# Performance work log

Hardware: AMD Instinct MI355X
Metric: run time of the kernel (lower is better)

The kernel has to match this reference:

```python
import jax, jax.numpy as jnp
import numpy as np

E = 8          # moe_num_experts
F = 4096       # ffn_hidden_size
D = 2048       # d_model
TOP_K = 2


def setup_inputs() -> dict:
    key = jax.random.key(0)
    k_x, k_r, k_w1, k_v1, k_w2 = jax.random.split(key, 5)
    scale = 0.02  # ~ normal initializer scale
    x = jax.random.normal(k_x, (2, 2048, D), dtype=jnp.float32)
    router_w = jax.random.normal(k_r, (D, E), dtype=jnp.float32) * scale
    w1 = jax.random.normal(k_w1, (E * F, D), dtype=jnp.float32) * scale
    v1 = jax.random.normal(k_v1, (E * F, D), dtype=jnp.float32) * scale
    w2 = jax.random.normal(k_w2, (E * F, D), dtype=jnp.float32) * scale
    return {"x": x, "router_w": router_w, "w1": w1, "v1": v1, "w2": w2}


def reference(x, router_w, w1, v1, w2):
    # --- Router: dense logits -> softmax (fp32) -> top-k -> L1 normalize ---
    logits = jnp.einsum("bsd,de->bse", x.astype(jnp.float32), router_w)
    weights = jax.nn.softmax(logits, axis=-1)                       # [B,S,E]
    top_weights, top_experts = jax.lax.top_k(weights, TOP_K)        # [B,S,K]
    # moe_normalize_expert_weights = 1 -> L1 norm
    top_weights = top_weights / jnp.sum(jnp.abs(top_weights), axis=-1, keepdims=True)
    top_weights = top_weights.astype(x.dtype)

    # --- Experts: dense per-expert GLU, masked combine (faithful to source) ---
    w1r = w1.reshape(E, F, D)
    v1r = v1.reshape(E, F, D)
    w2r = w2.reshape(E, F, D)
    out = jnp.zeros_like(x)
    for e in range(E):  # fixed small structural loop over experts
        x1 = jnp.einsum("bsd,fd->bsf", x, w1r[e])
        x2 = jnp.einsum("bsd,fd->bsf", x, v1r[e])
        h = jax.nn.silu(x1) * x2                                    # GLU
        y = jnp.einsum("bsf,fd->bsd", h, w2r[e])
        coef = jnp.sum((top_experts == e) * top_weights, axis=-1)[:, :, None]
        out = out + coef * y
    return out
```

## Files before the change

kernel.cpp:

```cpp
#include <hip/hip_runtime.h>
#include <cstdio>
#include <cstdint>

typedef _Float16 f16;
typedef _Float16 f16x8 __attribute__((ext_vector_type(8)));
typedef float f32x4 __attribute__((ext_vector_type(4)));

#define D_MODEL 2048
#define FFN     4096
#define FFN2    8192
#define NEXP    8
#define NTOK    4096
#define NENT    (NTOK*2)
#define BM      256
#define BN      256
#define BK      64
#define KSPLIT  4
#define KCHUNK  (FFN / KSPLIT)
#define MAX_ROWS  10240
#define MAX_TILES 40

__device__ __forceinline__ void gload_lds16(const void* g, void* l) {
  __builtin_amdgcn_global_load_lds(
      (const __attribute__((address_space(1))) void*)g,
      (__attribute__((address_space(3))) void*)l, 16, 0, 0);
}

template<int N> __device__ __forceinline__ void waitvm() {
  if constexpr (N == 0) asm volatile("s_waitcnt vmcnt(0)" ::: "memory");
  else if constexpr (N == 2) asm volatile("s_waitcnt vmcnt(2)" ::: "memory");
  else if constexpr (N == 4) asm volatile("s_waitcnt vmcnt(4)" ::: "memory");
  else if constexpr (N == 6) asm volatile("s_waitcnt vmcnt(6)" ::: "memory");
}

template<int LD>
__device__ __forceinline__ void stageA(const f16* aT, int k0, f16* AS, int mh, int tid) {
#pragma unroll
  for (int s = 0; s < 2; s++) {
    int o = s*8192 + tid*16;
    int rl = o >> 7;
    int ce = ((o & 127) ^ ((rl & 7) << 4)) >> 1;
    int arow = s*128 + mh*64 + (rl & 63);
    gload_lds16(aT + (size_t)arow * LD + k0 + ce,
                (char*)AS + mh*16384 + s*8192 + (tid & ~63)*16);
  }
}

template<int LD>
__device__ __forceinline__ void stageB(const f16* bT, int k0, f16* BS, int nh, int tid) {
#pragma unroll
  for (int s = 0; s < 2; s++) {
    int o = s*8192 + tid*16;
    int rl = o >> 7;
    int ce = ((o & 127) ^ ((rl & 7) << 4)) >> 1;
    int crow = (rl >> 5)*64 + nh*32 + (rl & 31);
    gload_lds16(bT + (size_t)crow * LD + k0 + ce,
                (char*)BS + nh*16384 + s*8192 + (tid & ~63)*16);
  }
}

__device__ __forceinline__ f16x8 fragLd(const f16* S, int row, int lane, int ks) {
  int kb = ks*64 + (lane >> 4)*16;
  int off = (row*128 + kb) ^ ((row & 7) << 4);
  return *(const f16x8*)((const char*)S + off);
}

template<int LD, int V0, int V1, int V3, bool SB0, bool SB1, bool SA1, bool SA0>
__device__ __forceinline__ void tile4(
    const f16* aT, const f16* bT, int k1, int k2,
    f16* ASc, f16* BSc, f16* ASn, f16* BSn,
    f32x4 (&acc)[8][4], f16x8 (&aF)[4][2], f16x8 (&bF)[2][2][2],
    int tid, int lane, int wrM, int wcN) {
#pragma unroll
  for (int mf = 0; mf < 4; mf++)
#pragma unroll
    for (int ks = 0; ks < 2; ks++)
      aF[mf][ks] = fragLd(ASc, wrM*64 + mf*16 + (lane & 15), lane, ks);
#pragma unroll
  for (int nf = 0; nf < 2; nf++)
#pragma unroll
    for (int ks = 0; ks < 2; ks++)
      bF[0][nf][ks] = fragLd(BSc, wcN*32 + nf*16 + (lane & 15), lane, ks);
  if constexpr (SB0) stageB<LD>(bT, k1, BSn, 0, tid);
  __builtin_amdgcn_s_barrier();
  __builtin_amdgcn_s_setprio(1);
#pragma unroll
  for (int mf = 0; mf < 4; mf++)
#pragma unroll
    for (int nf = 0; nf < 2; nf++)
#pragma unroll
      for (int ks = 0; ks < 2; ks++)
        acc[mf][nf] = __builtin_amdgcn_mfma_f32_16x16x32_f16(aF[mf][ks], bF[0][nf][ks], acc[mf][nf], 0, 0, 0);
  __builtin_amdgcn_s_setprio(0);
  waitvm<V0>();
  __builtin_amdgcn_s_barrier();
#pragma unroll
  for (int nf = 0; nf < 2; nf++)
#pragma unroll
    for (int ks = 0; ks < 2; ks++)
      bF[1][nf][ks] = fragLd(BSc, 128 + wcN*32 + nf*16 + (lane & 15), lane, ks);
  if constexpr (SB1) stageB<LD>(bT, k1, BSn, 1, tid);
  __builtin_amdgcn_s_barrier();
  __builtin_amdgcn_s_setprio(1);
#pragma unroll
  for (int mf = 0; mf < 4; mf++)
#pragma unroll
    for (int nf = 0; nf < 2; nf++)
#pragma unroll
      for (int ks = 0; ks < 2; ks++)
        acc[mf][2+nf] = __builtin_amdgcn_mfma_f32_16x16x32_f16(aF[mf][ks], bF[1][nf][ks], acc[mf][2+nf], 0, 0, 0);
  __builtin_amdgcn_s_setprio(0);
  waitvm<V1>();
  __builtin_amdgcn_s_barrier();
#pragma unroll
  for (int mf = 0; mf < 4; mf++)
#pragma unroll
    for (int ks = 0; ks < 2; ks++)
      aF[mf][ks] = fragLd(ASc, 128 + wrM*64 + mf*16 + (lane & 15), lane, ks);
  if constexpr (SA1) stageA<LD>(aT, k1, ASn, 1, tid);
  __builtin_amdgcn_s_barrier();
  __builtin_amdgcn_s_setprio(1);
#pragma unroll
  for (int mf = 0; mf < 4; mf++)
#pragma unroll
    for (int nf = 0; nf < 2; nf++)
#pragma unroll
      for (int ks = 0; ks < 2; ks++)
        acc[4+mf][nf] = __builtin_amdgcn_mfma_f32_16x16x32_f16(aF[mf][ks], bF[0][nf][ks], acc[4+mf][nf], 0, 0, 0);
  __builtin_amdgcn_s_setprio(0);
  __builtin_amdgcn_s_barrier();
  if constexpr (SA0) stageA<LD>(aT, k2, ASc, 0, tid);
  __builtin_amdgcn_s_barrier();
  __builtin_amdgcn_s_setprio(1);
#pragma unroll
  for (int mf = 0; mf < 4; mf++)
#pragma unroll
    for (int nf = 0; nf < 2; nf++)
#pragma unroll
      for (int ks = 0; ks < 2; ks++)
        acc[4+mf][2+nf] = __builtin_amdgcn_mfma_f32_16x16x32_f16(aF[mf][ks], bF[1][nf][ks], acc[4+mf][2+nf], 0, 0, 0);
  __builtin_amdgcn_s_setprio(0);
  waitvm<V3>();
  __builtin_amdgcn_s_barrier();
}


__global__ void zero_counts_kernel(int* counts) {
  if (threadIdx.x < NEXP) counts[threadIdx.x] = 0;
}

__global__ __launch_bounds__(64) void router_kernel(
    const float* __restrict__ x, const float* __restrict__ rw,
    int* counts, int* te, float* tw, int* trank) {
  int t = blockIdx.x;
  int lane = threadIdx.x;
  float acc[8] = {0.f,0.f,0.f,0.f,0.f,0.f,0.f,0.f};
  const float* xr = x + (size_t)t * D_MODEL;
  for (int d = lane; d < D_MODEL; d += 64) {
    float xv = xr[d];
    const float4* r4 = (const float4*)(rw + (size_t)d * NEXP);
    float4 a = r4[0], b = r4[1];
    acc[0] += xv*a.x; acc[1] += xv*a.y; acc[2] += xv*a.z; acc[3] += xv*a.w;
    acc[4] += xv*b.x; acc[5] += xv*b.y; acc[6] += xv*b.z; acc[7] += xv*b.w;
  }
#pragma unroll
  for (int off = 32; off > 0; off >>= 1) {
#pragma unroll
    for (int e = 0; e < 8; e++) acc[e] += __shfl_down(acc[e], off);
  }
  if (lane == 0) {
    int e0 = 0;
#pragma unroll
    for (int e = 1; e < 8; e++) if (acc[e] > acc[e0]) e0 = e;
    int e1 = (e0 == 0) ? 1 : 0;
#pragma unroll
    for (int e = 0; e < 8; e++) if (e != e0 && acc[e] > acc[e1]) e1 = e;
    float c0 = 1.0f / (1.0f + expf(acc[e1] - acc[e0]));
    float c1 = 1.0f - c0;
    int r0 = atomicAdd(&counts[e0], 1);
    int r1 = atomicAdd(&counts[e1], 1);
    te[t*2] = e0; te[t*2+1] = e1;
    tw[t*2] = c0; tw[t*2+1] = c1;
    trank[t*2] = r0; trank[t*2+1] = r1;
  }
}

__global__ void sched_kernel(const int* counts, int* offsets, int4* sched, int* nT) {
  if (threadIdx.x != 0 || blockIdx.x != 0) return;
  int off = 0, n = 0;
  for (int e = 0; e < NEXP; e++) {
    offsets[e] = off;
    int cnt = counts[e];
    int nt = (cnt + BM - 1) / BM;
    for (int i = 0; i < nt; i++) {
      sched[n] = make_int4(e, off + i*BM, min(BM, cnt - i*BM), 0);
      n++;
    }
    off += nt * BM;
  }
  offsets[NEXP] = off;
  *nT = n;
}

__global__ __launch_bounds__(256) void gather_kernel(
    const float* __restrict__ x, const int* __restrict__ te,
    const float* __restrict__ tw, const int* __restrict__ trank,
    const int* __restrict__ offsets, f16* __restrict__ xg,
    int* __restrict__ token_of, float* __restrict__ coefs) {
  int i = blockIdx.x;
  int t = i >> 1;
  int e = te[i];
  int slot = offsets[e] + trank[i];
  if (threadIdx.x == 0) { token_of[slot] = t; coefs[slot] = tw[i]; }
  const float4* src = (const float4*)(x + (size_t)t * D_MODEL);
  f16x8* dst = (f16x8*)(xg + (size_t)slot * D_MODEL);
  for (int j = threadIdx.x; j < D_MODEL/8; j += 256) {
    float4 v0 = src[j*2], v1 = src[j*2+1];
    f16x8 h;
    h[0]=(f16)v0.x; h[1]=(f16)v0.y; h[2]=(f16)v0.z; h[3]=(f16)v0.w;
    h[4]=(f16)v1.x; h[5]=(f16)v1.y; h[6]=(f16)v1.z; h[7]=(f16)v1.w;
    dst[j] = h;
  }
}

__global__ __launch_bounds__(256) void convert_ileave_kernel(
    const float* __restrict__ src, f16* __restrict__ dst, int parity) {
  int n8 = NEXP*FFN*D_MODEL/8;
  int stride = gridDim.x * 256;
  for (int i = blockIdx.x*256 + threadIdx.x; i < n8; i += stride) {
    int d8 = i & (D_MODEL/8 - 1);
    int fr_glob = i >> 8;
    int e = fr_glob >> 12;
    int fr = fr_glob & (FFN - 1);
    int cr = ((fr >> 4)*2 + parity)*16 + (fr & 15);
    float4 v0 = ((const float4*)src)[(size_t)i*2];
    float4 v1 = ((const float4*)src)[(size_t)i*2 + 1];
    f16x8 h;
    h[0]=(f16)v0.x; h[1]=(f16)v0.y; h[2]=(f16)v0.z; h[3]=(f16)v0.w;
    h[4]=(f16)v1.x; h[5]=(f16)v1.y; h[6]=(f16)v1.z; h[7]=(f16)v1.w;
    ((f16x8*)dst)[((size_t)e*FFN2 + cr)*(D_MODEL/8) + d8] = h;
  }
}

__global__ __launch_bounds__(256) void transpose_w2_kernel(
    const float* __restrict__ w2, f16* __restrict__ w2t) {
  __shared__ float tl[64][65];
  int e = blockIdx.z;
  int d0 = blockIdx.x * 64, f0 = blockIdx.y * 64;
  const float* src = w2 + (size_t)e * FFN * D_MODEL;
  int tid = threadIdx.x;
  int fr = tid >> 4, c4 = (tid & 15) * 4;
#pragma unroll
  for (int rr = 0; rr < 4; rr++) {
    float4 v = *(const float4*)(src + (size_t)(f0 + fr + rr*16) * D_MODEL + d0 + c4);
    tl[fr + rr*16][c4+0] = v.x; tl[fr + rr*16][c4+1] = v.y;
    tl[fr + rr*16][c4+2] = v.z; tl[fr + rr*16][c4+3] = v.w;
  }
  __syncthreads();
  int dr = tid >> 2, fg = (tid & 3) * 16;
  f16* dst = w2t + (size_t)e * D_MODEL * FFN + (size_t)(d0 + dr) * FFN + f0 + fg;
  f16 tmp[16];
#pragma unroll
  for (int j = 0; j < 16; j++) tmp[j] = (f16)tl[fg + j][dr];
  *(float4*)(dst)     = *(float4*)(tmp);
  *(float4*)(dst + 8) = *(float4*)(tmp + 8);
}

__global__ __launch_bounds__(512, 2) void phaseA_kernel(
    const f16* __restrict__ xg, const f16* __restrict__ w12h,
    f16* __restrict__ hbuf, const int4* __restrict__ sched, const int* __restrict__ nT) {
  int tile = blockIdx.y;
  if (tile >= *nT) return;
  int4 sc = sched[tile];
  int e = sc.x, row0 = sc.y;
  int fc0 = blockIdx.x * BN;

  __shared__ f16 AS[2][BM*BK];
  __shared__ f16 BS[2][BN*BK];

  int tid = threadIdx.x, lane = tid & 63, wid = tid >> 6;
  int wrM = wid >> 2, wcN = wid & 3;

  const f16* aT = xg  + (size_t)row0 * D_MODEL;
  const f16* bT = w12h + (size_t)e * FFN2 * D_MODEL + (size_t)fc0 * D_MODEL;

  f32x4 acc[8][4]; f16x8 aF[4][2]; f16x8 bF[2][2][2];
  f32x4 z4 = {0.f,0.f,0.f,0.f};
#pragma unroll
  for (int m = 0; m < 8; m++)
#pragma unroll
    for (int n = 0; n < 4; n++) acc[m][n] = z4;

  stageA<D_MODEL>(aT, 0, AS[0], 0, tid);
  stageB<D_MODEL>(bT, 0, BS[0], 0, tid);
  stageB<D_MODEL>(bT, 0, BS[0], 1, tid);
  stageA<D_MODEL>(aT, 0, AS[0], 1, tid);
  stageA<D_MODEL>(aT, BK, AS[1], 0, tid);
  waitvm<6>();
  __builtin_amdgcn_s_barrier();

  constexpr int NTILES = D_MODEL / BK;
  for (int t = 0; t + 2 < NTILES; t++) {
    int b = t & 1;
    tile4<D_MODEL,6,6,6,true,true,true,true>(aT, bT, (t+1)*BK, (t+2)*BK,
        AS[b], BS[b], AS[b^1], BS[b^1], acc, aF, bF, tid, lane, wrM, wcN);
  }
  { int b = (NTILES-2) & 1;
    tile4<D_MODEL,6,6,4,true,true,true,false>(aT, bT, (NTILES-1)*BK, 0,
        AS[b], BS[b], AS[b^1], BS[b^1], acc, aF, bF, tid, lane, wrM, wcN); }
  { int b = (NTILES-1) & 1;
    tile4<D_MODEL,2,0,-1,false,false,false,false>(aT, bT, 0, 0,
        AS[b], BS[b], AS[b^1], BS[b^1], acc, aF, bF, tid, lane, wrM, wcN); }

  int i15 = lane & 15, l4 = lane >> 4;
#pragma unroll
  for (int m = 0; m < 8; m++) {
    int rowl = wrM*128 + (m>>2)*64 + (m&3)*16 + l4*4;
#pragma unroll
    for (int nh = 0; nh < 2; nh++) {
      int f = (fc0 >> 1) + wcN*32 + nh*16 + i15;
      f16* hb = hbuf + (size_t)(row0 + rowl) * FFN + f;
#pragma unroll
      for (int q = 0; q < 4; q++) {
        float x1 = acc[m][nh*2+0][q], x2 = acc[m][nh*2+1][q];
        float hv = x1 / (1.0f + __expf(-x1)) * x2;
        hb[(size_t)q * FFN] = (f16)hv;
      }
    }
  }
}

__global__ __launch_bounds__(512, 2) void phaseB_kernel(
    const f16* __restrict__ hbuf, const f16* __restrict__ w2t,
    f16* __restrict__ yb0, f16* __restrict__ ybR,
    const int4* __restrict__ sched, const int* __restrict__ nT) {
  int tile = blockIdx.y;
  if (tile >= *nT) return;
  int4 sc = sched[tile];
  int e = sc.x, row0 = sc.y;
  int dc0 = blockIdx.x * BN;
  int z = blockIdx.z;

  __shared__ f16 AS[2][BM*BK];
  __shared__ f16 BS[2][BN*BK];

  int tid = threadIdx.x, lane = tid & 63, wid = tid >> 6;
  int wrM = wid >> 2, wcN = wid & 3;

  const f16* aT = hbuf + (size_t)row0 * FFN + z * KCHUNK;
  const f16* bT = w2t + (size_t)e * D_MODEL * FFN + (size_t)dc0 * FFN + z * KCHUNK;

  f32x4 acc[8][4]; f16x8 aF[4][2]; f16x8 bF[2][2][2];
  f32x4 z4 = {0.f,0.f,0.f,0.f};
#pragma unroll
  for (int m = 0; m < 8; m++)
#pragma unroll
    for (int n = 0; n < 4; n++) acc[m][n] = z4;

  stageA<FFN>(aT, 0, AS[0], 0, tid);
  stageB<FFN>(bT, 0, BS[0], 0, tid);
  stageB<FFN>(bT, 0, BS[0], 1, tid);
  stageA<FFN>(aT, 0, AS[0], 1, tid);
  stageA<FFN>(aT, BK, AS[1], 0, tid);
  waitvm<6>();
  __builtin_amdgcn_s_barrier();

  constexpr int NTILES = KCHUNK / BK;
  for (int t = 0; t + 2 < NTILES; t++) {
    int b = t & 1;
    tile4<FFN,6,6,6,true,true,true,true>(aT, bT, (t+1)*BK, (t+2)*BK,
        AS[b], BS[b], AS[b^1], BS[b^1], acc, aF, bF, tid, lane, wrM, wcN);
  }
  { int b = (NTILES-2) & 1;
    tile4<FFN,6,6,4,true,true,true,false>(aT, bT, (NTILES-1)*BK, 0,
        AS[b], BS[b], AS[b^1], BS[b^1], acc, aF, bF, tid, lane, wrM, wcN); }
  { int b = (NTILES-1) & 1;
    tile4<FFN,2,0,-1,false,false,false,false>(aT, bT, 0, 0,
        AS[b], BS[b], AS[b^1], BS[b^1], acc, aF, bF, tid, lane, wrM, wcN); }

  f16* yb = (z == 0) ? yb0 : (ybR + (size_t)(z-1) * MAX_ROWS * D_MODEL);
  int i15 = lane & 15, l4 = lane >> 4;
#pragma unroll
  for (int m = 0; m < 8; m++) {
#pragma unroll
    for (int q = 0; q < 4; q++) {
      int rl = wrM*128 + (m>>2)*64 + (m&3)*16 + l4*4 + q;
      f16* yrow = yb + (size_t)(row0 + rl) * D_MODEL + dc0 + wcN*64;
#pragma unroll
      for (int n = 0; n < 4; n++)
        yrow[(n>>1)*32 + (n&1)*16 + i15] = (f16)acc[m][n][q];
    }
  }
}

__global__ __launch_bounds__(256) void combine_kernel(
    const f16* __restrict__ yb0, const f16* __restrict__ ybR,
    const int* __restrict__ te, const float* __restrict__ tw,
    const int* __restrict__ trank, const int* __restrict__ offsets,
    float* __restrict__ out) {
  int t = blockIdx.x;
  int d8 = threadIdx.x;
  int s0 = offsets[te[2*t]]   + trank[2*t];
  int s1 = offsets[te[2*t+1]] + trank[2*t+1];
  float w0 = tw[2*t], w1 = tw[2*t+1];
  float sum[8] = {0.f,0.f,0.f,0.f,0.f,0.f,0.f,0.f};
#pragma unroll
  for (int z = 0; z < KSPLIT; z++) {
    const f16* yb = (z == 0) ? yb0 : (ybR + (size_t)(z-1) * MAX_ROWS * D_MODEL);
    f16x8 a = ((const f16x8*)(yb + (size_t)s0 * D_MODEL))[d8];
    f16x8 b = ((const f16x8*)(yb + (size_t)s1 * D_MODEL))[d8];
#pragma unroll
    for (int j = 0; j < 8; j++) sum[j] += w0 * (float)a[j] + w1 * (float)b[j];
  }
  float* o = out + (size_t)t * D_MODEL + d8*8;
  float4 o0 = {sum[0], sum[1], sum[2], sum[3]};
  float4 o1 = {sum[4], sum[5], sum[6], sum[7]};
  ((float4*)o)[0] = o0;
  ((float4*)o)[1] = o1;
}

extern "C" void kernel_launch(void* const* d_in, const int* in_sizes, int n_in,
                              void* d_out, int out_size, void* d_ws, size_t ws_size,
                              hipStream_t stream) {
  const float* x  = (const float*)d_in[0];
  const float* rw = (const float*)d_in[1];
  const float* w1 = (const float*)d_in[2];
  const float* v1 = (const float*)d_in[3];
  const float* w2 = (const float*)d_in[4];
  float* out = (float*)d_out;

  char* p = (char*)d_ws;
  auto alloc = [&](size_t bytes) {
    char* r = p;
    p += (bytes + 255) & ~(size_t)255;
    return r;
  };
  int*   counts   = (int*)  alloc(NEXP * 4);
  int*   nT       = (int*)  alloc(4);
  int*   offsets  = (int*)  alloc((NEXP + 1) * 4);
  int*   te       = (int*)  alloc(NENT * 4);
  float* tw       = (float*)alloc(NENT * 4);
  int*   trank    = (int*)  alloc(NENT * 4);
  int*   token_of = (int*)  alloc(MAX_ROWS * 4);
  float* coefs    = (float*)alloc(MAX_ROWS * 4);
  int4*  sched    = (int4*) alloc(MAX_TILES * 16);
  f16*   xg       = (f16*)  alloc((size_t)MAX_ROWS * D_MODEL * 2);
  f16*   hbuf     = (f16*)  alloc((size_t)MAX_ROWS * FFN * 2);
  f16*   w12h     = (f16*)  alloc((size_t)NEXP * FFN2 * D_MODEL * 2);
  f16*   w2t      = (f16*)  alloc((size_t)NEXP * FFN * D_MODEL * 2);
  size_t needed = (size_t)(p - (char*)d_ws);
  if (needed > ws_size) {
    fprintf(stderr, "kernel_launch: ws too small: need %zu, have %zu\n", needed, ws_size);
    return;
  }
  f16* yb0 = xg;
  f16* ybR = w12h;

  zero_counts_kernel<<<1, 64, 0, stream>>>(counts);
  router_kernel<<<NTOK, 64, 0, stream>>>(x, rw, counts, te, tw, trank);
  sched_kernel<<<1, 1, 0, stream>>>(counts, offsets, sched, nT);
  gather_kernel<<<NENT, 256, 0, stream>>>(x, te, tw, trank, offsets, xg, token_of, coefs);
  convert_ileave_kernel<<<4096, 256, 0, stream>>>(w1, w12h, 0);
  convert_ileave_kernel<<<4096, 256, 0, stream>>>(v1, w12h, 1);
  transpose_w2_kernel<<<dim3(D_MODEL/64, FFN/64, NEXP), 256, 0, stream>>>(w2, w2t);
  phaseA_kernel<<<dim3(FFN2/BN, MAX_TILES), 512, 0, stream>>>(xg, w12h, hbuf, sched, nT);
  phaseB_kernel<<<dim3(D_MODEL/BN, MAX_TILES, KSPLIT), 512, 0, stream>>>(hbuf, w2t, yb0, ybR, sched, nT);
  combine_kernel<<<NTOK, 256, 0, stream>>>(yb0, ybR, te, tw, trank, offsets, out);
}
```

Baseline: 897.8 us.

## Make MoE GEMM kernels persistent with atomic work queue and simplified K pipeline

Phase A and phase B GEMMs now launch a fixed 256 blocks that pull work units from a global atomic counter, instead of launching a grid sized for the maximum tile count in which surplus blocks exit early. The K-loop pipeline is also restructured: each tile iteration stages the whole next-next A and B tile into the current buffer late in the iteration, replacing the earlier interleaved half-tile staging. The goal is to cut launch and early-exit block overhead and to balance load across CUs. In exchange, each work unit now starts with a cold pipeline prologue, per-unit atomic and syncthreads overhead is added, and the prefetch distance changes.

```diff
diff --git a/kernel.cpp b/kernel.cpp
--- a/kernel.cpp
+++ b/kernel.cpp
@@ -17,6 +17,8 @@
 #define BK      64
 #define KSPLIT  4
 #define KCHUNK  (FFN / KSPLIT)
+#define NTA     (D_MODEL / BK)
+#define NTB     (KCHUNK / BK)
 #define MAX_ROWS  10240
 #define MAX_TILES 40
 
@@ -28,35 +30,37 @@
 
 template<int N> __device__ __forceinline__ void waitvm() {
   if constexpr (N == 0) asm volatile("s_waitcnt vmcnt(0)" ::: "memory");
-  else if constexpr (N == 2) asm volatile("s_waitcnt vmcnt(2)" ::: "memory");
-  else if constexpr (N == 4) asm volatile("s_waitcnt vmcnt(4)" ::: "memory");
-  else if constexpr (N == 6) asm volatile("s_waitcnt vmcnt(6)" ::: "memory");
+  else if constexpr (N == 8) asm volatile("s_waitcnt vmcnt(8)" ::: "memory");
 }
 
 template<int LD>
-__device__ __forceinline__ void stageA(const f16* aT, int k0, f16* AS, int mh, int tid) {
-#pragma unroll
-  for (int s = 0; s < 2; s++) {
-    int o = s*8192 + tid*16;
-    int rl = o >> 7;
-    int ce = ((o & 127) ^ ((rl & 7) << 4)) >> 1;
-    int arow = s*128 + mh*64 + (rl & 63);
-    gload_lds16(aT + (size_t)arow * LD + k0 + ce,
-                (char*)AS + mh*16384 + s*8192 + (tid & ~63)*16);
-  }
+__device__ __forceinline__ void stageA(const f16* aT, int k0, f16* AS, int tid) {
+#pragma unroll
+  for (int mh = 0; mh < 2; mh++)
+#pragma unroll
+    for (int s = 0; s < 2; s++) {
+      int o = s*8192 + tid*16;
+      int rl = o >> 7;
+      int ce = ((o & 127) ^ ((rl & 7) << 4)) >> 1;
+      int arow = s*128 + mh*64 + (rl & 63);
+      gload_lds16(aT + (size_t)arow * LD + k0 + ce,
+                  (char*)AS + mh*16384 + s*8192 + (tid & ~63)*16);
+    }
 }
 
 template<int LD>
-__device__ __forceinline__ void stageB(const f16* bT, int k0, f16* BS, int nh, int tid) {
-#pragma unroll
-  for (int s = 0; s < 2; s++) {
-    int o = s*8192 + tid*16;
-    int rl = o >> 7;
-    int ce = ((o & 127) ^ ((rl & 7) << 4)) >> 1;
-    int crow = (rl >> 5)*64 + nh*32 + (rl & 31);
-    gload_lds16(bT + (size_t)crow * LD + k0 + ce,
-                (char*)BS + nh*16384 + s*8192 + (tid & ~63)*16);
-  }
+__device__ __forceinline__ void stageB(const f16* bT, int k0, f16* BS, int tid) {
+#pragma unroll
+  for (int nh = 0; nh < 2; nh++)
+#pragma unroll
+    for (int s = 0; s < 2; s++) {
+      int o = s*8192 + tid*16;
+      int rl = o >> 7;
+      int ce = ((o & 127) ^ ((rl & 7) << 4)) >> 1;
+      int crow = (rl >> 5)*64 + nh*32 + (rl & 31);
+      gload_lds16(bT + (size_t)crow * LD + k0 + ce,
+                  (char*)BS + nh*16384 + s*8192 + (tid & ~63)*16);
+    }
 }
 
 __device__ __forceinline__ f16x8 fragLd(const f16* S, int row, int lane, int ks) {
@@ -65,10 +69,23 @@
   return *(const f16x8*)((const char*)S + off);
 }
 
-template<int LD, int V0, int V1, int V3, bool SB0, bool SB1, bool SA1, bool SA0>
-__device__ __forceinline__ void tile4(
-    const f16* aT, const f16* bT, int k1, int k2,
-    f16* ASc, f16* BSc, f16* ASn, f16* BSn,
+__device__ __forceinline__ void quad(
+    f32x4 (&acc)[8][4], int mo, int no,
+    f16x8 (&aF)[4][2], f16x8 (&bFh)[2][2]) {
+#pragma unroll
+  for (int mf = 0; mf < 4; mf++)
+#pragma unroll
+    for (int nf = 0; nf < 2; nf++)
+#pragma unroll
+      for (int ks = 0; ks < 2; ks++)
+        acc[mo+mf][no+nf] = __builtin_amdgcn_mfma_f32_16x16x32_f16(
+            aF[mf][ks], bFh[nf][ks], acc[mo+mf][no+nf], 0, 0, 0);
+}
+
+template<int LD, int VEND, bool STG>
+__device__ __forceinline__ void tileK(
+    const f16* aT, const f16* bT, int k2,
+    f16* ASc, f16* BSc,
     f32x4 (&acc)[8][4], f16x8 (&aF)[4][2], f16x8 (&bF)[2][2][2],
     int tid, int lane, int wrM, int wcN) {
 #pragma unroll
@@ -81,72 +98,45 @@
 #pragma unroll
     for (int ks = 0; ks < 2; ks++)
       bF[0][nf][ks] = fragLd(BSc, wcN*32 + nf*16 + (lane & 15), lane, ks);
-  if constexpr (SB0) stageB<LD>(bT, k1, BSn, 0, tid);
   __builtin_amdgcn_s_barrier();
   __builtin_amdgcn_s_setprio(1);
-#pragma unroll
-  for (int mf = 0; mf < 4; mf++)
-#pragma unroll
-    for (int nf = 0; nf < 2; nf++)
-#pragma unroll
-      for (int ks = 0; ks < 2; ks++)
-        acc[mf][nf] = __builtin_amdgcn_mfma_f32_16x16x32_f16(aF[mf][ks], bF[0][nf][ks], acc[mf][nf], 0, 0, 0);
+  quad(acc, 0, 0, aF, bF[0]);
   __builtin_amdgcn_s_setprio(0);
-  waitvm<V0>();
   __builtin_amdgcn_s_barrier();
 #pragma unroll
   for (int nf = 0; nf < 2; nf++)
 #pragma unroll
     for (int ks = 0; ks < 2; ks++)
       bF[1][nf][ks] = fragLd(BSc, 128 + wcN*32 + nf*16 + (lane & 15), lane, ks);
-  if constexpr (SB1) stageB<LD>(bT, k1, BSn, 1, tid);
   __builtin_amdgcn_s_barrier();
   __builtin_amdgcn_s_setprio(1);
-#pragma unroll
-  for (int mf = 0; mf < 4; mf++)
-#pragma unroll
-    for (int nf = 0; nf < 2; nf++)
-#pragma unroll
-      for (int ks = 0; ks < 2; ks++)
-        acc[mf][2+nf] = __builtin_amdgcn_mfma_f32_16x16x32_f16(aF[mf][ks], bF[1][nf][ks], acc[mf][2+nf], 0, 0, 0);
+  quad(acc, 0, 2, aF, bF[1]);
   __builtin_amdgcn_s_setprio(0);
-  waitvm<V1>();
   __builtin_amdgcn_s_barrier();
 #pragma unroll
   for (int mf = 0; mf < 4; mf++)
 #pragma unroll
     for (int ks = 0; ks < 2; ks++)
       aF[mf][ks] = fragLd(ASc, 128 + wrM*64 + mf*16 + (lane & 15), lane, ks);
-  if constexpr (SA1) stageA<LD>(aT, k1, ASn, 1, tid);
+  if constexpr (STG) stageB<LD>(bT, k2, BSc, tid);
   __builtin_amdgcn_s_barrier();
   __builtin_amdgcn_s_setprio(1);
-#pragma unroll
-  for (int mf = 0; mf < 4; mf++)
-#pragma unroll
-    for (int nf = 0; nf < 2; nf++)
-#pragma unroll
-      for (int ks = 0; ks < 2; ks++)
-        acc[4+mf][nf] = __builtin_amdgcn_mfma_f32_16x16x32_f16(aF[mf][ks], bF[0][nf][ks], acc[4+mf][nf], 0, 0, 0);
+  quad(acc, 4, 0, aF, bF[0]);
   __builtin_amdgcn_s_setprio(0);
   __builtin_amdgcn_s_barrier();
-  if constexpr (SA0) stageA<LD>(aT, k2, ASc, 0, tid);
+  if constexpr (STG) stageA<LD>(aT, k2, ASc, tid);
   __builtin_amdgcn_s_barrier();
   __builtin_amdgcn_s_setprio(1);
-#pragma unroll
-  for (int mf = 0; mf < 4; mf++)
-#pragma unroll
-    for (int nf = 0; nf < 2; nf++)
-#pragma unroll
-      for (int ks = 0; ks < 2; ks++)
-        acc[4+mf][2+nf] = __builtin_amdgcn_mfma_f32_16x16x32_f16(aF[mf][ks], bF[1][nf][ks], acc[4+mf][2+nf], 0, 0, 0);
+  quad(acc, 4, 2, aF, bF[1]);
   __builtin_amdgcn_s_setprio(0);
-  waitvm<V3>();
-  __builtin_amdgcn_s_barrier();
-}
-
-
-__global__ void zero_counts_kernel(int* counts) {
+  waitvm<VEND>();
+  __builtin_amdgcn_s_barrier();
+}
+
+
+__global__ void zero_counts_kernel(int* counts, int* wctr) {
   if (threadIdx.x < NEXP) counts[threadIdx.x] = 0;
+  if (threadIdx.x < 2) wctr[threadIdx.x] = 0;
 }
 
 __global__ __launch_bounds__(64) void router_kernel(
@@ -268,63 +258,65 @@
 
 __global__ __launch_bounds__(512, 2) void phaseA_kernel(
     const f16* __restrict__ xg, const f16* __restrict__ w12h,
-    f16* __restrict__ hbuf, const int4* __restrict__ sched, const int* __restrict__ nT) {
-  int tile = blockIdx.y;
-  if (tile >= *nT) return;
-  int4 sc = sched[tile];
-  int e = sc.x, row0 = sc.y;
-  int fc0 = blockIdx.x * BN;
-
+    f16* __restrict__ hbuf, const int4* __restrict__ sched, const int* __restrict__ nT,
+    int* __restrict__ wctr) {
   __shared__ f16 AS[2][BM*BK];
   __shared__ f16 BS[2][BN*BK];
+  __shared__ int s_u;
 
   int tid = threadIdx.x, lane = tid & 63, wid = tid >> 6;
   int wrM = wid >> 2, wcN = wid & 3;
-
-  const f16* aT = xg  + (size_t)row0 * D_MODEL;
-  const f16* bT = w12h + (size_t)e * FFN2 * D_MODEL + (size_t)fc0 * D_MODEL;
-
-  f32x4 acc[8][4]; f16x8 aF[4][2]; f16x8 bF[2][2][2];
-  f32x4 z4 = {0.f,0.f,0.f,0.f};
-#pragma unroll
-  for (int m = 0; m < 8; m++)
-#pragma unroll
-    for (int n = 0; n < 4; n++) acc[m][n] = z4;
-
-  stageA<D_MODEL>(aT, 0, AS[0], 0, tid);
-  stageB<D_MODEL>(bT, 0, BS[0], 0, tid);
-  stageB<D_MODEL>(bT, 0, BS[0], 1, tid);
-  stageA<D_MODEL>(aT, 0, AS[0], 1, tid);
-  stageA<D_MODEL>(aT, BK, AS[1], 0, tid);
-  waitvm<6>();
-  __builtin_amdgcn_s_barrier();
-
-  constexpr int NTILES = D_MODEL / BK;
-  for (int t = 0; t + 2 < NTILES; t++) {
-    int b = t & 1;
-    tile4<D_MODEL,6,6,6,true,true,true,true>(aT, bT, (t+1)*BK, (t+2)*BK,
-        AS[b], BS[b], AS[b^1], BS[b^1], acc, aF, bF, tid, lane, wrM, wcN);
-  }
-  { int b = (NTILES-2) & 1;
-    tile4<D_MODEL,6,6,4,true,true,true,false>(aT, bT, (NTILES-1)*BK, 0,
-        AS[b], BS[b], AS[b^1], BS[b^1], acc, aF, bF, tid, lane, wrM, wcN); }
-  { int b = (NTILES-1) & 1;
-    tile4<D_MODEL,2,0,-1,false,false,false,false>(aT, bT, 0, 0,
-        AS[b], BS[b], AS[b^1], BS[b^1], acc, aF, bF, tid, lane, wrM, wcN); }
-
-  int i15 = lane & 15, l4 = lane >> 4;
-#pragma unroll
-  for (int m = 0; m < 8; m++) {
-    int rowl = wrM*128 + (m>>2)*64 + (m&3)*16 + l4*4;
-#pragma unroll
-    for (int nh = 0; nh < 2; nh++) {
-      int f = (fc0 >> 1) + wcN*32 + nh*16 + i15;
-      f16* hb = hbuf + (size_t)(row0 + rowl) * FFN + f;
-#pragma unroll
-      for (int q = 0; q < 4; q++) {
-        float x1 = acc[m][nh*2+0][q], x2 = acc[m][nh*2+1][q];
-        float hv = x1 / (1.0f + __expf(-x1)) * x2;
-        hb[(size_t)q * FFN] = (f16)hv;
+  int nW = (*nT) * (FFN2 / BN);
+
+  for (;;) {
+    if (tid == 0) s_u = atomicAdd(wctr, 1);
+    __syncthreads();
+    int u = s_u;
+    if (u >= nW) break;
+    int tile = u >> 5;
+    int fc0 = (u & 31) * BN;
+    int4 sc = sched[tile];
+    int e = sc.x, row0 = sc.y;
+
+    const f16* aT = xg  + (size_t)row0 * D_MODEL;
+    const f16* bT = w12h + (size_t)e * FFN2 * D_MODEL + (size_t)fc0 * D_MODEL;
+
+    f32x4 acc[8][4]; f16x8 aF[4][2]; f16x8 bF[2][2][2];
+    f32x4 z4 = {0.f,0.f,0.f,0.f};
+#pragma unroll
+    for (int m = 0; m < 8; m++)
+#pragma unroll
+      for (int n = 0; n < 4; n++) acc[m][n] = z4;
+
+    stageA<D_MODEL>(aT, 0, AS[0], tid);
+    stageB<D_MODEL>(bT, 0, BS[0], tid);
+    stageA<D_MODEL>(aT, BK, AS[1], tid);
+    stageB<D_MODEL>(bT, BK, BS[1], tid);
+    waitvm<8>();
+    __builtin_amdgcn_s_barrier();
+
+    for (int t = 0; t < NTA - 2; t++)
+      tileK<D_MODEL,8,true>(aT, bT, (t+2)*BK, AS[t&1], BS[t&1],
+                            acc, aF, bF, tid, lane, wrM, wcN);
+    tileK<D_MODEL,0,false>(aT, bT, 0, AS[(NTA-2)&1], BS[(NTA-2)&1],
+                           acc, aF, bF, tid, lane, wrM, wcN);
+    tileK<D_MODEL,-1,false>(aT, bT, 0, AS[(NTA-1)&1], BS[(NTA-1)&1],
+                            acc, aF, bF, tid, lane, wrM, wcN);
+
+    int i15 = lane & 15, l4 = lane >> 4;
+#pragma unroll
+    for (int m = 0; m < 8; m++) {
+      int rowl = wrM*128 + (m>>2)*64 + (m&3)*16 + l4*4;
+#pragma unroll
+      for (int nh = 0; nh < 2; nh++) {
+        int f = (fc0 >> 1) + wcN*32 + nh*16 + i15;
+        f16* hb = hbuf + (size_t)(row0 + rowl) * FFN + f;
+#pragma unroll
+        for (int q = 0; q < 4; q++) {
+          float x1 = acc[m][nh*2+0][q], x2 = acc[m][nh*2+1][q];
+          float hv = x1 / (1.0f + __expf(-x1)) * x2;
+          hb[(size_t)q * FFN] = (f16)hv;
+        }
       }
     }
   }
@@ -333,62 +325,64 @@
 __global__ __launch_bounds__(512, 2) void phaseB_kernel(
     const f16* __restrict__ hbuf, const f16* __restrict__ w2t,
     f16* __restrict__ yb0, f16* __restrict__ ybR,
-    const int4* __restrict__ sched, const int* __restrict__ nT) {
-  int tile = blockIdx.y;
-  if (tile >= *nT) return;
-  int4 sc = sched[tile];
-  int e = sc.x, row0 = sc.y;
-  int dc0 = blockIdx.x * BN;
-  int z = blockIdx.z;
-
+    const int4* __restrict__ sched, const int* __restrict__ nT,
+    int* __restrict__ wctr) {
   __shared__ f16 AS[2][BM*BK];
   __shared__ f16 BS[2][BN*BK];
+  __shared__ int s_u;
 
   int tid = threadIdx.x, lane = tid & 63, wid = tid >> 6;
   int wrM = wid >> 2, wcN = wid & 3;
-
-  const f16* aT = hbuf + (size_t)row0 * FFN + z * KCHUNK;
-  const f16* bT = w2t + (size_t)e * D_MODEL * FFN + (size_t)dc0 * FFN + z * KCHUNK;
-
-  f32x4 acc[8][4]; f16x8 aF[4][2]; f16x8 bF[2][2][2];
-  f32x4 z4 = {0.f,0.f,0.f,0.f};
-#pragma unroll
-  for (int m = 0; m < 8; m++)
-#pragma unroll
-    for (int n = 0; n < 4; n++) acc[m][n] = z4;
-
-  stageA<FFN>(aT, 0, AS[0], 0, tid);
-  stageB<FFN>(bT, 0, BS[0], 0, tid);
-  stageB<FFN>(bT, 0, BS[0], 1, tid);
-  stageA<FFN>(aT, 0, AS[0], 1, tid);
-  stageA<FFN>(aT, BK, AS[1], 0, tid);
-  waitvm<6>();
-  __builtin_amdgcn_s_barrier();
-
-  constexpr int NTILES = KCHUNK / BK;
-  for (int t = 0; t + 2 < NTILES; t++) {
-    int b = t & 1;
-    tile4<FFN,6,6,6,true,true,true,true>(aT, bT, (t+1)*BK, (t+2)*BK,
-        AS[b], BS[b], AS[b^1], BS[b^1], acc, aF, bF, tid, lane, wrM, wcN);
-  }
-  { int b = (NTILES-2) & 1;
-    tile4<FFN,6,6,4,true,true,true,false>(aT, bT, (NTILES-1)*BK, 0,
-        AS[b], BS[b], AS[b^1], BS[b^1], acc, aF, bF, tid, lane, wrM, wcN); }
-  { int b = (NTILES-1) & 1;
-    tile4<FFN,2,0,-1,false,false,false,false>(aT, bT, 0, 0,
-        AS[b], BS[b], AS[b^1], BS[b^1], acc, aF, bF, tid, lane, wrM, wcN); }
-
-  f16* yb = (z == 0) ? yb0 : (ybR + (size_t)(z-1) * MAX_ROWS * D_MODEL);
-  int i15 = lane & 15, l4 = lane >> 4;
-#pragma unroll
-  for (int m = 0; m < 8; m++) {
-#pragma unroll
-    for (int q = 0; q < 4; q++) {
-      int rl = wrM*128 + (m>>2)*64 + (m&3)*16 + l4*4 + q;
-      f16* yrow = yb + (size_t)(row0 + rl) * D_MODEL + dc0 + wcN*64;
-#pragma unroll
-      for (int n = 0; n < 4; n++)
-        yrow[(n>>1)*32 + (n&1)*16 + i15] = (f16)acc[m][n][q];
+  int nW = (*nT) * (D_MODEL / BN) * KSPLIT;
+
+  for (;;) {
+    if (tid == 0) s_u = atomicAdd(wctr, 1);
+    __syncthreads();
+    int u = s_u;
+    if (u >= nW) break;
+    int z = u & 3;
+    int dc0 = ((u >> 2) & 7) * BN;
+    int tile = u >> 5;
+    int4 sc = sched[tile];
+    int e = sc.x, row0 = sc.y;
+
+    const f16* aT = hbuf + (size_t)row0 * FFN + z * KCHUNK;
+    const f16* bT = w2t + (size_t)e * D_MODEL * FFN + (size_t)dc0 * FFN + z * KCHUNK;
+
+    f32x4 acc[8][4]; f16x8 aF[4][2]; f16x8 bF[2][2][2];
+    f32x4 z4 = {0.f,0.f,0.f,0.f};
+#pragma unroll
+    for (int m = 0; m < 8; m++)
+#pragma unroll
+      for (int n = 0; n < 4; n++) acc[m][n] = z4;
+
+    stageA<FFN>(aT, 0, AS[0], tid);
+    stageB<FFN>(bT, 0, BS[0], tid);
+    stageA<FFN>(aT, BK, AS[1], tid);
+    stageB<FFN>(bT, BK, BS[1], tid);
+    waitvm<8>();
+    __builtin_amdgcn_s_barrier();
+
+    for (int t = 0; t < NTB - 2; t++)
+      tileK<FFN,8,true>(aT, bT, (t+2)*BK, AS[t&1], BS[t&1],
+                        acc, aF, bF, tid, lane, wrM, wcN);
+    tileK<FFN,0,false>(aT, bT, 0, AS[(NTB-2)&1], BS[(NTB-2)&1],
+                       acc, aF, bF, tid, lane, wrM, wcN);
+    tileK<FFN,-1,false>(aT, bT, 0, AS[(NTB-1)&1], BS[(NTB-1)&1],
+                        acc, aF, bF, tid, lane, wrM, wcN);
+
+    f16* yb = (z == 0) ? yb0 : (ybR + (size_t)(z-1) * MAX_ROWS * D_MODEL);
+    int i15 = lane & 15, l4 = lane >> 4;
+#pragma unroll
+    for (int m = 0; m < 8; m++) {
+#pragma unroll
+      for (int q = 0; q < 4; q++) {
+        int rl = wrM*128 + (m>>2)*64 + (m&3)*16 + l4*4 + q;
+        f16* yrow = yb + (size_t)(row0 + rl) * D_MODEL + dc0 + wcN*64;
+#pragma unroll
+        for (int n = 0; n < 4; n++)
+          yrow[(n>>1)*32 + (n&1)*16 + i15] = (f16)acc[m][n][q];
+      }
     }
   }
 }
@@ -436,6 +430,7 @@
     return r;
   };
   int*   counts   = (int*)  alloc(NEXP * 4);
+  int*   wctr     = (int*)  alloc(2 * 4);
   int*   nT       = (int*)  alloc(4);
   int*   offsets  = (int*)  alloc((NEXP + 1) * 4);
   int*   te       = (int*)  alloc(NENT * 4);
@@ -456,14 +451,14 @@
   f16* yb0 = xg;
   f16* ybR = w12h;
 
-  zero_counts_kernel<<<1, 64, 0, stream>>>(counts);
+  zero_counts_kernel<<<1, 64, 0, stream>>>(counts, wctr);
   router_kernel<<<NTOK, 64, 0, stream>>>(x, rw, counts, te, tw, trank);
   sched_kernel<<<1, 1, 0, stream>>>(counts, offsets, sched, nT);
   gather_kernel<<<NENT, 256, 0, stream>>>(x, te, tw, trank, offsets, xg, token_of, coefs);
   convert_ileave_kernel<<<4096, 256, 0, stream>>>(w1, w12h, 0);
   convert_ileave_kernel<<<4096, 256, 0, stream>>>(v1, w12h, 1);
   transpose_w2_kernel<<<dim3(D_MODEL/64, FFN/64, NEXP), 256, 0, stream>>>(w2, w2t);
-  phaseA_kernel<<<dim3(FFN2/BN, MAX_TILES), 512, 0, stream>>>(xg, w12h, hbuf, sched, nT);
-  phaseB_kernel<<<dim3(D_MODEL/BN, MAX_TILES, KSPLIT), 512, 0, stream>>>(hbuf, w2t, yb0, ybR, sched, nT);
+  phaseA_kernel<<<256, 512, 0, stream>>>(xg, w12h, hbuf, sched, nT, &wctr[0]);
+  phaseB_kernel<<<256, 512, 0, stream>>>(hbuf, w2t, yb0, ybR, sched, nT, &wctr[1]);
   combine_kernel<<<NTOK, 256, 0, stream>>>(yb0, ybR, te, tw, trank, offsets, out);
 }
```

Result: slower. 1.013 ms (+12.8%).

## Fuse w1/v1 conversion into one kernel and XCD-swizzle GEMM workgroup mapping

Applied to the files above, without the earlier changes.

Merges the two fp32-to-fp16 interleave kernels for w1 and v1 into a single launch that writes both halves of each interleaved row pair. Remaps the phaseA and phaseB workgroup indices so that consecutive logical tiles, which share the same expert weights and row block, are placed on the same XCD. This aims to improve L2 reuse of weight and activation tiles across the 8 XCDs and to cut one kernel launch. The swizzle assumes the round-robin XCD dispatch order and relies on grid dimensions matching the hardcoded 32- and 8-wide tile decompositions.

```diff
diff --git a/kernel.cpp b/kernel.cpp
--- a/kernel.cpp
+++ b/kernel.cpp
@@ -223,8 +223,9 @@
   }
 }
 
-__global__ __launch_bounds__(256) void convert_ileave_kernel(
-    const float* __restrict__ src, f16* __restrict__ dst, int parity) {
+__global__ __launch_bounds__(256) void convert_both_kernel(
+    const float* __restrict__ w1, const float* __restrict__ v1,
+    f16* __restrict__ dst) {
   int n8 = NEXP*FFN*D_MODEL/8;
   int stride = gridDim.x * 256;
   for (int i = blockIdx.x*256 + threadIdx.x; i < n8; i += stride) {
@@ -232,13 +233,19 @@
     int fr_glob = i >> 8;
     int e = fr_glob >> 12;
     int fr = fr_glob & (FFN - 1);
-    int cr = ((fr >> 4)*2 + parity)*16 + (fr & 15);
-    float4 v0 = ((const float4*)src)[(size_t)i*2];
-    float4 v1 = ((const float4*)src)[(size_t)i*2 + 1];
-    f16x8 h;
-    h[0]=(f16)v0.x; h[1]=(f16)v0.y; h[2]=(f16)v0.z; h[3]=(f16)v0.w;
-    h[4]=(f16)v1.x; h[5]=(f16)v1.y; h[6]=(f16)v1.z; h[7]=(f16)v1.w;
-    ((f16x8*)dst)[((size_t)e*FFN2 + cr)*(D_MODEL/8) + d8] = h;
+    int crbase = ((fr >> 4)*2)*16 + (fr & 15);
+    float4 a0 = ((const float4*)w1)[(size_t)i*2];
+    float4 a1 = ((const float4*)w1)[(size_t)i*2 + 1];
+    float4 b0 = ((const float4*)v1)[(size_t)i*2];
+    float4 b1 = ((const float4*)v1)[(size_t)i*2 + 1];
+    f16x8 ha, hb;
+    ha[0]=(f16)a0.x; ha[1]=(f16)a0.y; ha[2]=(f16)a0.z; ha[3]=(f16)a0.w;
+    ha[4]=(f16)a1.x; ha[5]=(f16)a1.y; ha[6]=(f16)a1.z; ha[7]=(f16)a1.w;
+    hb[0]=(f16)b0.x; hb[1]=(f16)b0.y; hb[2]=(f16)b0.z; hb[3]=(f16)b0.w;
+    hb[4]=(f16)b1.x; hb[5]=(f16)b1.y; hb[6]=(f16)b1.z; hb[7]=(f16)b1.w;
+    size_t base = ((size_t)e*FFN2 + crbase)*(D_MODEL/8) + d8;
+    ((f16x8*)dst)[base] = ha;
+    ((f16x8*)dst)[base + 16*(D_MODEL/8)] = hb;
   }
 }
 
@@ -269,11 +276,16 @@
 __global__ __launch_bounds__(512, 2) void phaseA_kernel(
     const f16* __restrict__ xg, const f16* __restrict__ w12h,
     f16* __restrict__ hbuf, const int4* __restrict__ sched, const int* __restrict__ nT) {
-  int tile = blockIdx.y;
+  int nwg = gridDim.x * gridDim.y;
+  int flat = blockIdx.x + gridDim.x * blockIdx.y;
+  int q = nwg >> 3, r = nwg & 7;
+  int xcd = flat & 7, loc = flat >> 3;
+  int swz = (xcd < r ? xcd*(q+1) : r*(q+1) + (xcd-r)*q) + loc;
+  int tile = swz >> 5;
   if (tile >= *nT) return;
+  int fc0 = (swz & 31) * BN;
   int4 sc = sched[tile];
   int e = sc.x, row0 = sc.y;
-  int fc0 = blockIdx.x * BN;
 
   __shared__ f16 AS[2][BM*BK];
   __shared__ f16 BS[2][BN*BK];
@@ -321,10 +333,10 @@
       int f = (fc0 >> 1) + wcN*32 + nh*16 + i15;
       f16* hb = hbuf + (size_t)(row0 + rowl) * FFN + f;
 #pragma unroll
-      for (int q = 0; q < 4; q++) {
-        float x1 = acc[m][nh*2+0][q], x2 = acc[m][nh*2+1][q];
+      for (int q2 = 0; q2 < 4; q2++) {
+        float x1 = acc[m][nh*2+0][q2], x2 = acc[m][nh*2+1][q2];
         float hv = x1 / (1.0f + __expf(-x1)) * x2;
-        hb[(size_t)q * FFN] = (f16)hv;
+        hb[(size_t)q2 * FFN] = (f16)hv;
       }
     }
   }
@@ -334,12 +346,18 @@
     const f16* __restrict__ hbuf, const f16* __restrict__ w2t,
     f16* __restrict__ yb0, f16* __restrict__ ybR,
     const int4* __restrict__ sched, const int* __restrict__ nT) {
-  int tile = blockIdx.y;
+  int nwg = gridDim.x * gridDim.y * gridDim.z;
+  int flat = blockIdx.x + gridDim.x * (blockIdx.y + gridDim.y * blockIdx.z);
+  int q = nwg >> 3, r = nwg & 7;
+  int xcd = flat & 7, loc = flat >> 3;
+  int swz = (xcd < r ? xcd*(q+1) : r*(q+1) + (xcd-r)*q) + loc;
+  int z = swz / (MAX_TILES * 8);
+  int rem = swz - z * (MAX_TILES * 8);
+  int tile = rem >> 3;
   if (tile >= *nT) return;
+  int dc0 = (rem & 7) * BN;
   int4 sc = sched[tile];
   int e = sc.x, row0 = sc.y;
-  int dc0 = blockIdx.x * BN;
-  int z = blockIdx.z;
 
   __shared__ f16 AS[2][BM*BK];
   __shared__ f16 BS[2][BN*BK];
@@ -383,12 +401,12 @@
 #pragma unroll
   for (int m = 0; m < 8; m++) {
 #pragma unroll
-    for (int q = 0; q < 4; q++) {
-      int rl = wrM*128 + (m>>2)*64 + (m&3)*16 + l4*4 + q;
+    for (int q2 = 0; q2 < 4; q2++) {
+      int rl = wrM*128 + (m>>2)*64 + (m&3)*16 + l4*4 + q2;
       f16* yrow = yb + (size_t)(row0 + rl) * D_MODEL + dc0 + wcN*64;
 #pragma unroll
       for (int n = 0; n < 4; n++)
-        yrow[(n>>1)*32 + (n&1)*16 + i15] = (f16)acc[m][n][q];
+        yrow[(n>>1)*32 + (n&1)*16 + i15] = (f16)acc[m][n][q2];
     }
   }
 }
@@ -460,8 +478,7 @@
   router_kernel<<<NTOK, 64, 0, stream>>>(x, rw, counts, te, tw, trank);
   sched_kernel<<<1, 1, 0, stream>>>(counts, offsets, sched, nT);
   gather_kernel<<<NENT, 256, 0, stream>>>(x, te, tw, trank, offsets, xg, token_of, coefs);
-  convert_ileave_kernel<<<4096, 256, 0, stream>>>(w1, w12h, 0);
-  convert_ileave_kernel<<<4096, 256, 0, stream>>>(v1, w12h, 1);
+  convert_both_kernel<<<4096, 256, 0, stream>>>(w1, v1, w12h);
   transpose_w2_kernel<<<dim3(D_MODEL/64, FFN/64, NEXP), 256, 0, stream>>>(w2, w2t);
   phaseA_kernel<<<dim3(FFN2/BN, MAX_TILES), 512, 0, stream>>>(xg, w12h, hbuf, sched, nT);
   phaseB_kernel<<<dim3(D_MODEL/BN, MAX_TILES, KSPLIT), 512, 0, stream>>>(hbuf, w2t, yb0, ybR, sched, nT);
```

Measured after the change: 958.4 us. 1.07x slower.
